# Performance work log

Measured on AMD Instinct MI355X. Metric: run time of the kernel, lower is better.

Reference implementation:

```python
import jax, jax.numpy as jnp
import numpy as np

N = 1024   # codeword length (variable nodes)
M_CN = 512 # check nodes
DV = 3     # variable-node degree
DC = 6     # check-node degree
E = N * DV # edges = 3072
B = 128    # batch of codewords
CLIP = 0.999999


def _build_masks():
    rng = np.random.default_rng(0)
    vn = np.repeat(np.arange(N), DV)                    # [E] variable node of each edge
    cn = rng.permutation(np.repeat(np.arange(M_CN), DC))  # [E] check node of each edge
    off = ~np.eye(E, dtype=bool)
    vn2cn = ((cn[:, None] == cn[None, :]) & off).astype(np.float32)  # [E,E] same check, excl self
    cn2vn = ((vn[:, None] == vn[None, :]) & off).astype(np.float32)  # [E,E] same vn, excl self
    onehot = (vn[:, None] == np.arange(N)[None, :]).astype(np.float32)  # [E,N]
    first = np.clip(vn2cn @ onehot, 0.0, 1.0)           # [E,N] vns in same check, excl own edge
    out_mask = onehot.T.copy()                          # [N,E]
    bias_mat = onehot.T.copy()                          # [N,E] routes LLR[v] to its edges
    return first, cn2vn, vn2cn, out_mask, bias_mat


def setup_inputs() -> dict:
    key = jax.random.key(0)
    x = jax.random.normal(key, (B, N), dtype=jnp.float32) * 2.0  # channel LLRs
    first, cn2vn, vn2cn, out_mask, bias_mat = _build_masks()
    return {
        "x": x,
        "first_mask": jnp.asarray(first),
        "cn2vn_mask": jnp.asarray(cn2vn),
        "vn2cn_mask": jnp.asarray(vn2cn),
        "out_mask": jnp.asarray(out_mask),
        "bias_mat": jnp.asarray(bias_mat),
    }


def _cn_update(x, mask):
    # Faithful to CnUpdateLayer: out[:,i] = prod_j of (x[:,j]*mask[i,j]) over nonzero
    # masked entries (masked-off or exactly-zero entries treated as 1), and 0 if no
    # nonzero masked entry. Computed fused in log/sign domain via matmuls instead of
    # the original per-column Python loop.
    nz = (x != 0.0)
    logabs = jnp.where(nz, jnp.log(jnp.abs(jnp.where(nz, x, 1.0))), 0.0)  # [B,I]
    neg = ((x < 0.0) & nz).astype(x.dtype)
    s = logabs @ mask.T                          # [B,O] sum log|x_j| over masked j
    negcnt = neg @ mask.T                        # [B,O] number of negative factors
    cnt = nz.astype(x.dtype) @ mask.T            # [B,O] number of nonzero factors
    sign = 1.0 - 2.0 * (negcnt % 2.0)
    return jnp.where(cnt > 0.0, sign * jnp.exp(s), 0.0)


def reference(x, first_mask, cn2vn_mask, vn2cn_mask, out_mask, bias_mat):
    llr = x  # Channel_LLR; bias_scaling_vectors are identity matrices (no-ops)
    bias = llr @ bias_mat  # [B,E], reused each iteration

    def cn_to_llr(h):
        return 2.0 * jnp.arctanh(jnp.clip(h, -CLIP, CLIP))

    h = jnp.tanh(0.5 * x)
    h = cn_to_llr(_cn_update(h, first_mask))          # fc0
    out1 = jax.nn.sigmoid(h @ out_mask.T + llr)

    h = jnp.tanh(0.5 * (h @ cn2vn_mask.T + bias))     # fc1
    h = cn_to_llr(_cn_update(h, vn2cn_mask))          # fc2
    out2 = jax.nn.sigmoid(h @ out_mask.T + llr)

    h = jnp.tanh(0.5 * (h @ cn2vn_mask.T + bias))     # fc3
    h = cn_to_llr(_cn_update(h, vn2cn_mask))          # fc4
    out3 = jax.nn.sigmoid(h @ out_mask.T + llr)

    h = jnp.tanh(0.5 * (h @ cn2vn_mask.T + bias))     # fc5
    h = cn_to_llr(_cn_update(h, vn2cn_mask))          # fc6
    out4 = jax.nn.sigmoid(h @ out_mask.T + llr)

    h = jnp.tanh(0.5 * (h @ cn2vn_mask.T + bias))     # fc7
    h = cn_to_llr(_cn_update(h, vn2cn_mask))          # fc8
    out5 = jax.nn.sigmoid(h @ out_mask.T + llr)       # fc9 (out_mask) + identity-scaled LLR

    return (out5, out4, out3, out2, out1)
```

## Files before the change

kernel.cpp:

```cpp
#include <hip/hip_runtime.h>
#include <math.h>

namespace {
constexpr int kN = 1024;
constexpr int kE = 3072;
constexpr int kB = 128;
constexpr float kClip = 0.999999f;
}

#define RCP(x) __builtin_amdgcn_rcpf(x)

__global__ __launch_bounds__(256) void extract_partners_kernel(
    const uint4* __restrict__ mask, unsigned long long* __restrict__ part) {
  __shared__ int slots[4][8];
  const int wave = threadIdx.x >> 6, lane = threadIdx.x & 63;
  const int row = blockIdx.x * 4 + wave;
  const uint4* rp = mask + (size_t)row * (kE / 4);
  const int it0 = (row + 1) >> 8;

  uint4 vals[12];
#pragma unroll
  for (int it = 0; it < 12; ++it)
    if (it >= it0) vals[it] = rp[it * 64 + lane];

  const unsigned long long lt = (1ULL << lane) - 1ULL;
  int cnt = 0;
#pragma unroll
  for (int it = 0; it < 12; ++it) {
    if (it < it0) continue;
    uint4 v = vals[it];
    const int idx = it * 256 + lane * 4;
    const bool b0 = (v.x != 0u) & (idx + 0 > row);
    const bool b1 = (v.y != 0u) & (idx + 1 > row);
    const bool b2 = (v.z != 0u) & (idx + 2 > row);
    const bool b3 = (v.w != 0u) & (idx + 3 > row);
    unsigned long long m0 = __ballot(b0);
    unsigned long long m1 = __ballot(b1);
    unsigned long long m2 = __ballot(b2);
    unsigned long long m3 = __ballot(b3);
    int before = cnt + __popcll(m0 & lt) + __popcll(m1 & lt) +
                 __popcll(m2 & lt) + __popcll(m3 & lt);
    int own = 0;
    if (b0) slots[wave][min(before + own, 7)] = idx + 0;
    own += (int)((m0 >> lane) & 1ULL);
    if (b1) slots[wave][min(before + own, 7)] = idx + 1;
    own += (int)((m1 >> lane) & 1ULL);
    if (b2) slots[wave][min(before + own, 7)] = idx + 2;
    own += (int)((m2 >> lane) & 1ULL);
    if (b3) slots[wave][min(before + own, 7)] = idx + 3;
    cnt += __popcll(m0) + __popcll(m1) + __popcll(m2) + __popcll(m3);
  }
  __syncthreads();
  if (cnt == 5 && lane < 6) {
    int g[6];
    g[0] = row;
#pragma unroll
    for (int i = 0; i < 5; ++i) g[i + 1] = slots[wave][i];
    unsigned long long pk = 0;
    int sh = 0;
#pragma unroll
    for (int i = 0; i < 6; ++i)
      if (i != lane) {
        pk |= (unsigned long long)(g[i] & 0xFFF) << sh;
        sh += 12;
      }
    part[g[lane]] = pk;
  }
}

__global__ __launch_bounds__(1024) void bp_kernel(
    const float* __restrict__ x, const unsigned long long* __restrict__ part,
    float* __restrict__ out) {
  __shared__ float tmV[kN];
  __shared__ float tmE[2][kE];
  const int b = blockIdx.x;
  const int tid = threadIdx.x;

  int idx[3][5];
#pragma unroll
  for (int i = 0; i < 3; ++i) {
    const unsigned long long pk = part[3 * tid + i];
#pragma unroll
    for (int j = 0; j < 5; ++j) idx[i][j] = (int)((pk >> (12 * j)) & 0xFFF);
  }

  const float l = x[(size_t)b * kN + tid];
  const float E = __expf(l);
  tmV[tid] = (E - 1.0f) * RCP(E + 1.0f);
  __syncthreads();

  float y[3];
#pragma unroll
  for (int i = 0; i < 3; ++i) {
    const int q0 = idx[i][0] / 3, q1 = idx[i][1] / 3, q2 = idx[i][2] / 3,
              q3 = idx[i][3] / 3, q4 = idx[i][4] / 3;
    float prod = tmV[q0];
    const float f1 = tmV[q1], f2 = tmV[q2], f3 = tmV[q3], f4 = tmV[q4];
    prod *= (q1 == q0) ? 1.0f : f1;
    prod *= (q2 == q0 || q2 == q1) ? 1.0f : f2;
    prod *= (q3 == q0 || q3 == q1 || q3 == q2) ? 1.0f : f3;
    prod *= (q4 == q0 || q4 == q1 || q4 == q2 || q4 == q3) ? 1.0f : f4;
    y[i] = fminf(fmaxf(prod, -kClip), kClip);
  }

  float* ob = out + (size_t)b * kN + tid;

#define OUT_VN(slot, wbuf)                                                 \
  {                                                                        \
    const float a0 = 1.0f + y[0], a1 = 1.0f + y[1], a2 = 1.0f + y[2];      \
    const float s0 = 1.0f - y[0], s1 = 1.0f - y[1], s2 = 1.0f - y[2];      \
    const float Nn = E * a0 * a1 * a2;                                     \
    const float Dd = s0 * s1 * s2;                                         \
    ob[(size_t)(slot) * kB * kN] = Nn * RCP(Nn + Dd);                      \
    const float n0 = E * a1 * a2, d0 = s1 * s2;                            \
    const float n1 = E * a0 * a2, d1 = s0 * s2;                            \
    const float n2 = E * a0 * a1, d2 = s0 * s1;                            \
    (wbuf)[3 * tid + 0] = (n0 - d0) * RCP(n0 + d0);                        \
    (wbuf)[3 * tid + 1] = (n1 - d1) * RCP(n1 + d1);                        \
    (wbuf)[3 * tid + 2] = (n2 - d2) * RCP(n2 + d2);                        \
  }

#define CN(rbuf)                                                           \
  {                                                                        \
    _Pragma("unroll") for (int i = 0; i < 3; ++i) {                        \
      const float p = (rbuf)[idx[i][0]] * (rbuf)[idx[i][1]] *              \
                      (rbuf)[idx[i][2]] * (rbuf)[idx[i][3]] *              \
                      (rbuf)[idx[i][4]];                                   \
      y[i] = fminf(fmaxf(p, -kClip), kClip);                               \
    }                                                                      \
  }

  OUT_VN(4, tmE[0]);
  __syncthreads();
  CN(tmE[0]);
  OUT_VN(3, tmE[1]);
  __syncthreads();
  CN(tmE[1]);
  OUT_VN(2, tmE[0]);
  __syncthreads();
  CN(tmE[0]);
  OUT_VN(1, tmE[1]);
  __syncthreads();
  CN(tmE[1]);
  {
    const float a0 = 1.0f + y[0], a1 = 1.0f + y[1], a2 = 1.0f + y[2];
    const float s0 = 1.0f - y[0], s1 = 1.0f - y[1], s2 = 1.0f - y[2];
    const float Nn = E * a0 * a1 * a2;
    const float Dd = s0 * s1 * s2;
    ob[0] = Nn * RCP(Nn + Dd);
  }
#undef OUT_VN
#undef CN
}

extern "C" void kernel_launch(void* const* d_in, const int* in_sizes, int n_in,
                              void* d_out, int out_size, void* d_ws, size_t ws_size,
                              hipStream_t stream) {
  const float* x = (const float*)d_in[0];
  const float* vn2cn = (const float*)d_in[3];
  unsigned long long* part = (unsigned long long*)d_ws;
  float* out = (float*)d_out;

  hipLaunchKernelGGL(extract_partners_kernel, dim3(kE / 4), dim3(256), 0, stream,
                     (const uint4*)vn2cn, part);
  hipLaunchKernelGGL(bp_kernel, dim3(kB), dim3(1024), 0, stream, x, part, out);
}
```

Measured before the change: 17.96 us.

## Duplicate each codeword's BP across two 512-thread blocks splitting output writes

Launches two blocks per codeword with 512 threads each, and each thread now handles two variable nodes. Both blocks redundantly run the full belief propagation, and they split the five output stores between them by parity. The goal is to spread work over more CUs (256 blocks instead of 128) and halve the global store traffic per block. The cost is doubled compute and shared-memory work and more registers per thread.

```diff
diff --git a/kernel.cpp b/kernel.cpp
--- a/kernel.cpp
+++ b/kernel.cpp
@@ -68,86 +68,104 @@
   }
 }
 
-__global__ __launch_bounds__(1024) void bp_kernel(
+__global__ __launch_bounds__(512) void bp_kernel(
     const float* __restrict__ x, const unsigned long long* __restrict__ part,
     float* __restrict__ out) {
   __shared__ float tmV[kN];
   __shared__ float tmE[2][kE];
-  const int b = blockIdx.x;
+  const int b = blockIdx.x >> 1;
+  const int h = blockIdx.x & 1;
   const int tid = threadIdx.x;
 
-  int idx[3][5];
+  int idx[2][3][5];
+  float E[2];
 #pragma unroll
-  for (int i = 0; i < 3; ++i) {
-    const unsigned long long pk = part[3 * tid + i];
+  for (int u = 0; u < 2; ++u) {
+    const int v = tid + u * 512;
 #pragma unroll
-    for (int j = 0; j < 5; ++j) idx[i][j] = (int)((pk >> (12 * j)) & 0xFFF);
+    for (int i = 0; i < 3; ++i) {
+      const unsigned long long pk = part[3 * v + i];
+#pragma unroll
+      for (int j = 0; j < 5; ++j)
+        idx[u][i][j] = (int)((pk >> (12 * j)) & 0xFFF);
+    }
+    const float l = x[(size_t)b * kN + v];
+    E[u] = __expf(l);
+    tmV[v] = (E[u] - 1.0f) * RCP(E[u] + 1.0f);
   }
-
-  const float l = x[(size_t)b * kN + tid];
-  const float E = __expf(l);
-  tmV[tid] = (E - 1.0f) * RCP(E + 1.0f);
   __syncthreads();
 
-  float y[3];
+  float y[2][3];
 #pragma unroll
-  for (int i = 0; i < 3; ++i) {
-    const int q0 = idx[i][0] / 3, q1 = idx[i][1] / 3, q2 = idx[i][2] / 3,
-              q3 = idx[i][3] / 3, q4 = idx[i][4] / 3;
-    float prod = tmV[q0];
-    const float f1 = tmV[q1], f2 = tmV[q2], f3 = tmV[q3], f4 = tmV[q4];
-    prod *= (q1 == q0) ? 1.0f : f1;
-    prod *= (q2 == q0 || q2 == q1) ? 1.0f : f2;
-    prod *= (q3 == q0 || q3 == q1 || q3 == q2) ? 1.0f : f3;
-    prod *= (q4 == q0 || q4 == q1 || q4 == q2 || q4 == q3) ? 1.0f : f4;
-    y[i] = fminf(fmaxf(prod, -kClip), kClip);
-  }
+  for (int u = 0; u < 2; ++u)
+#pragma unroll
+    for (int i = 0; i < 3; ++i) {
+      const int q0 = idx[u][i][0] / 3, q1 = idx[u][i][1] / 3,
+                q2 = idx[u][i][2] / 3, q3 = idx[u][i][3] / 3,
+                q4 = idx[u][i][4] / 3;
+      float prod = tmV[q0];
+      const float f1 = tmV[q1], f2 = tmV[q2], f3 = tmV[q3], f4 = tmV[q4];
+      prod *= (q1 == q0) ? 1.0f : f1;
+      prod *= (q2 == q0 || q2 == q1) ? 1.0f : f2;
+      prod *= (q3 == q0 || q3 == q1 || q3 == q2) ? 1.0f : f3;
+      prod *= (q4 == q0 || q4 == q1 || q4 == q2 || q4 == q3) ? 1.0f : f4;
+      y[u][i] = fminf(fmaxf(prod, -kClip), kClip);
+    }
 
-  float* ob = out + (size_t)b * kN + tid;
-
-#define OUT_VN(slot, wbuf)                                                 \
-  {                                                                        \
-    const float a0 = 1.0f + y[0], a1 = 1.0f + y[1], a2 = 1.0f + y[2];      \
-    const float s0 = 1.0f - y[0], s1 = 1.0f - y[1], s2 = 1.0f - y[2];      \
-    const float Nn = E * a0 * a1 * a2;                                     \
-    const float Dd = s0 * s1 * s2;                                         \
-    ob[(size_t)(slot) * kB * kN] = Nn * RCP(Nn + Dd);                      \
-    const float n0 = E * a1 * a2, d0 = s1 * s2;                            \
-    const float n1 = E * a0 * a2, d1 = s0 * s2;                            \
-    const float n2 = E * a0 * a1, d2 = s0 * s1;                            \
-    (wbuf)[3 * tid + 0] = (n0 - d0) * RCP(n0 + d0);                        \
-    (wbuf)[3 * tid + 1] = (n1 - d1) * RCP(n1 + d1);                        \
-    (wbuf)[3 * tid + 2] = (n2 - d2) * RCP(n2 + d2);                        \
+#define OUT_VN(slot, doit, wbuf)                                           \
+  _Pragma("unroll") for (int u = 0; u < 2; ++u) {                          \
+    const float a0 = 1.0f + y[u][0], a1 = 1.0f + y[u][1],                  \
+                a2 = 1.0f + y[u][2];                                       \
+    const float s0 = 1.0f - y[u][0], s1 = 1.0f - y[u][1],                  \
+                s2 = 1.0f - y[u][2];                                       \
+    const float Ee = E[u];                                                 \
+    if (doit) {                                                            \
+      const float Nn = Ee * a0 * a1 * a2;                                  \
+      const float Dd = s0 * s1 * s2;                                       \
+      out[(size_t)(slot) * kB * kN + (size_t)b * kN + tid + u * 512] =     \
+          Nn * RCP(Nn + Dd);                                               \
+    }                                                                      \
+    const int e0 = 3 * (tid + u * 512);                                    \
+    const float n0 = Ee * a1 * a2, d0 = s1 * s2;                           \
+    const float n1 = Ee * a0 * a2, d1 = s0 * s2;                           \
+    const float n2 = Ee * a0 * a1, d2 = s0 * s1;                           \
+    (wbuf)[e0 + 0] = (n0 - d0) * RCP(n0 + d0);                             \
+    (wbuf)[e0 + 1] = (n1 - d1) * RCP(n1 + d1);                             \
+    (wbuf)[e0 + 2] = (n2 - d2) * RCP(n2 + d2);                             \
   }
 
 #define CN(rbuf)                                                           \
-  {                                                                        \
-    _Pragma("unroll") for (int i = 0; i < 3; ++i) {                        \
-      const float p = (rbuf)[idx[i][0]] * (rbuf)[idx[i][1]] *              \
-                      (rbuf)[idx[i][2]] * (rbuf)[idx[i][3]] *              \
-                      (rbuf)[idx[i][4]];                                   \
-      y[i] = fminf(fmaxf(p, -kClip), kClip);                               \
-    }                                                                      \
+  _Pragma("unroll") for (int u = 0; u < 2; ++u)                            \
+      _Pragma("unroll") for (int i = 0; i < 3; ++i) {                      \
+    const float p = (rbuf)[idx[u][i][0]] * (rbuf)[idx[u][i][1]] *          \
+                    (rbuf)[idx[u][i][2]] * (rbuf)[idx[u][i][3]] *          \
+                    (rbuf)[idx[u][i][4]];                                  \
+    y[u][i] = fminf(fmaxf(p, -kClip), kClip);                              \
   }
 
-  OUT_VN(4, tmE[0]);
+  OUT_VN(4, h == 1, tmE[0]);
   __syncthreads();
   CN(tmE[0]);
-  OUT_VN(3, tmE[1]);
+  OUT_VN(3, h == 0, tmE[1]);
   __syncthreads();
   CN(tmE[1]);
-  OUT_VN(2, tmE[0]);
+  OUT_VN(2, h == 1, tmE[0]);
   __syncthreads();
   CN(tmE[0]);
-  OUT_VN(1, tmE[1]);
+  OUT_VN(1, h == 0, tmE[1]);
   __syncthreads();
   CN(tmE[1]);
-  {
-    const float a0 = 1.0f + y[0], a1 = 1.0f + y[1], a2 = 1.0f + y[2];
-    const float s0 = 1.0f - y[0], s1 = 1.0f - y[1], s2 = 1.0f - y[2];
-    const float Nn = E * a0 * a1 * a2;
-    const float Dd = s0 * s1 * s2;
-    ob[0] = Nn * RCP(Nn + Dd);
+  if (h == 1) {
+#pragma unroll
+    for (int u = 0; u < 2; ++u) {
+      const float a0 = 1.0f + y[u][0], a1 = 1.0f + y[u][1],
+                  a2 = 1.0f + y[u][2];
+      const float s0 = 1.0f - y[u][0], s1 = 1.0f - y[u][1],
+                  s2 = 1.0f - y[u][2];
+      const float Nn = E[u] * a0 * a1 * a2;
+      const float Dd = s0 * s1 * s2;
+      out[(size_t)b * kN + tid + u * 512] = Nn * RCP(Nn + Dd);
+    }
   }
 #undef OUT_VN
 #undef CN
@@ -163,5 +181,5 @@
 
   hipLaunchKernelGGL(extract_partners_kernel, dim3(kE / 4), dim3(256), 0, stream,
                      (const uint4*)vn2cn, part);
-  hipLaunchKernelGGL(bp_kernel, dim3(kB), dim3(1024), 0, stream, x, part, out);
+  hipLaunchKernelGGL(bp_kernel, dim3(2 * kB), dim3(512), 0, stream, x, part, out);
 }
```

Result: slower. 19.22 us (+7.0%).
